# Performance work log

Hardware: AMD Instinct MI355X
Metric: run time of the kernel (lower is better)

The kernel has to match this reference:

```python
import jax, jax.numpy as jnp
import numpy as np

N_NODES = 50000
N_EDGES = 500000
NEG_SLOPE = 0.2  # PyG GATConv default leaky_relu slope
EPS = 1e-16


def gat_conv(x, src, dst, W, a_src, a_dst, b, heads, ch):
    """PyG-style GATConv (concat=True), self-loops assumed already in src/dst."""
    n = x.shape[0]
    h = (x @ W).reshape(n, heads, ch)                      # [N,H,C]
    alpha_s = jnp.sum(h * a_src, axis=-1)                  # [N,H]
    alpha_d = jnp.sum(h * a_dst, axis=-1)                  # [N,H]
    e = jax.nn.leaky_relu(alpha_s[src] + alpha_d[dst], NEG_SLOPE)  # [E,H]
    m = jax.ops.segment_max(e, dst, num_segments=n)        # [N,H] segment softmax (stable)
    m = jnp.where(jnp.isfinite(m), m, 0.0)
    ex = jnp.exp(e - m[dst])
    den = jax.ops.segment_sum(ex, dst, num_segments=n)
    alpha = ex / (den[dst] + EPS)                          # [E,H]
    msg = h[src] * alpha[..., None]                        # [E,H,C] gather->weight
    out = jax.ops.segment_sum(msg, dst, num_segments=n)    # [N,H,C] scatter-add
    return out.reshape(n, heads * ch) + b


def setup_inputs() -> dict:
    key = jax.random.key(0)
    ks = jax.random.split(key, 11)
    s = 0.05
    return {
        "edge_index": jax.random.randint(ks[0], (2, N_EDGES), 0, N_NODES, dtype=jnp.int32),
        "batch_size": 8,
        "node_emb": jax.random.normal(ks[1], (N_NODES, 64), jnp.float32),
        "W1": jax.random.normal(ks[2], (64, 512), jnp.float32) * s,
        "att_src1": jax.random.normal(ks[3], (4, 128), jnp.float32) * s,
        "att_dst1": jax.random.normal(ks[4], (4, 128), jnp.float32) * s,
        "b1": jax.random.normal(ks[5], (512,), jnp.float32) * s,
        "W2": jax.random.normal(ks[6], (512, 256), jnp.float32) * s,
        "att_src2": jax.random.normal(ks[7], (1, 256), jnp.float32) * s,
        "att_dst2": jax.random.normal(ks[8], (1, 256), jnp.float32) * s,
        "b2": jax.random.normal(ks[9], (256,), jnp.float32) * s,
    }


def reference(edge_index, batch_size, node_emb, W1, att_src1, att_dst1, b1,
              W2, att_src2, att_dst2, b2):
    # add self-loops (PyG GATConv default add_self_loops=True)
    loops = jnp.arange(N_NODES, dtype=edge_index.dtype)
    src = jnp.concatenate([edge_index[0], loops])
    dst = jnp.concatenate([edge_index[1], loops])
    x = gat_conv(node_emb, src, dst, W1, att_src1, att_dst1, b1, heads=4, ch=128)
    x = jax.nn.elu(x)  # dropout inactive at eval
    x = gat_conv(x, src, dst, W2, att_src2, att_dst2, b2, heads=1, ch=256)
    g = jnp.mean(x, axis=0, keepdims=True)                 # [1, 256]
    return jnp.broadcast_to(g, (batch_size, g.shape[1]))
```

## Files before the change

### kernel.cpp

```cpp
#include <hip/hip_runtime.h>
#include <cstdint>

#define N_NODES 50000
#define N_EDGES 500000
#define ET (N_NODES + N_EDGES)
#define EBLK 2149
#define NEBLK8 1563

typedef unsigned short u16;
typedef unsigned int   u32;
typedef __attribute__((ext_vector_type(8))) short short8;
typedef __attribute__((ext_vector_type(4))) float f32x4;

__device__ __forceinline__ float bf2f(u16 s) { return __uint_as_float((u32)s << 16); }
__device__ __forceinline__ u16 f2bf(float f) {
  u32 u = __float_as_uint(f);
  u32 r = (u + 0x7FFFu + ((u >> 16) & 1u)) >> 16;
  return (u16)r;
}
__device__ __forceinline__ void unpack8(uint4 u, float* f) {
  f[0] = __uint_as_float(u.x << 16); f[1] = __uint_as_float(u.x & 0xffff0000u);
  f[2] = __uint_as_float(u.y << 16); f[3] = __uint_as_float(u.y & 0xffff0000u);
  f[4] = __uint_as_float(u.z << 16); f[5] = __uint_as_float(u.z & 0xffff0000u);
  f[6] = __uint_as_float(u.w << 16); f[7] = __uint_as_float(u.w & 0xffff0000u);
}
__device__ __forceinline__ float lrelu(float v) { return v >= 0.f ? v : 0.2f * v; }

__device__ __forceinline__ int detect_fp32(const u16* __restrict__ ne) {
  int lane = threadIdx.x & 63;
  int bad = 0;
  #pragma unroll
  for (int j = 0; j < 2; ++j) {
    float v = fabsf(bf2f(ne[lane * 2 + j * 128]));
    bad += (!(v < 16.0f)) ? 1 : 0;
  }
  #pragma unroll
  for (int off = 32; off >= 1; off >>= 1) bad += __shfl_xor(bad, off, 64);
  return bad > 16;
}

__global__ __launch_bounds__(256) void k_prep(const int* __restrict__ ei,
                                              int* __restrict__ deg,
                                              const void* __restrict__ ne_src,
                                              u16* __restrict__ ne_b,
                                              const void* __restrict__ w1src,
                                              u16* __restrict__ W1t,
                                              const void* __restrict__ w2src,
                                              u16* __restrict__ W2t,
                                              const void* s0, const void* s1,
                                              const void* s2, const void* s3,
                                              const void* s4, const void* s5,
                                              float* d0, float* d1, float* d2,
                                              float* d3, float* d4, float* d5) {
  int b = blockIdx.x, tid = threadIdx.x;
  if (b < EBLK) {
    int e = b * 256 + tid;
    if (e < ET) {
      int d = (e < N_EDGES) ? ei[N_EDGES + e] : (e - N_EDGES);
      atomicAdd(&deg[d], 1);
    }
    return;
  }
  int fp32 = detect_fp32((const u16*)ne_src);
  b -= EBLK;
  if (b < NEBLK8) {
    int idx = b * 256 + tid;
    if (idx < 400000) {
      if (fp32) {
        const float4* f4 = (const float4*)ne_src;
        float4 a = f4[idx * 2], c = f4[idx * 2 + 1];
        uint4 o;
        o.x = (u32)f2bf(a.x) | ((u32)f2bf(a.y) << 16);
        o.y = (u32)f2bf(a.z) | ((u32)f2bf(a.w) << 16);
        o.z = (u32)f2bf(c.x) | ((u32)f2bf(c.y) << 16);
        o.w = (u32)f2bf(c.z) | ((u32)f2bf(c.w) << 16);
        ((uint4*)ne_b)[idx] = o;
      } else {
        ((uint4*)ne_b)[idx] = ((const uint4*)ne_src)[idx];
      }
    }
    return;
  }
  b -= NEBLK8;
  if (b < 640) {
    int i = b * 256 + tid;
    if (i < 32768) {
      int n = i >> 6, k = i & 63;
      W1t[i] = fp32 ? f2bf(((const float*)w1src)[k * 512 + n])
                    : ((const u16*)w1src)[k * 512 + n];
    } else {
      int j = i - 32768;
      int n = j >> 9, k = j & 511;
      W2t[j] = fp32 ? f2bf(((const float*)w2src)[k * 256 + n])
                    : ((const u16*)w2src)[k * 256 + n];
    }
    return;
  }
  b -= 640;
  {
    int i = b * 256 + tid;
    const void* s; float* d; int j;
    if      (i < 512)  { s = s0; d = d0; j = i; }
    else if (i < 1024) { s = s1; d = d1; j = i - 512; }
    else if (i < 1536) { s = s2; d = d2; j = i - 1024; }
    else if (i < 1792) { s = s3; d = d3; j = i - 1536; }
    else if (i < 2048) { s = s4; d = d4; j = i - 1792; }
    else if (i < 2304) { s = s5; d = d5; j = i - 2048; }
    else return;
    d[j] = fp32 ? ((const float*)s)[j] : bf2f(((const u16*)s)[j]);
  }
}

__global__ void k_vab(const u16* __restrict__ W1t,
                      const float* __restrict__ as1v, const float* __restrict__ ad1v,
                      float* __restrict__ va_s, float* __restrict__ va_d,
                      const u16* __restrict__ W2t,
                      const float* __restrict__ as2v, const float* __restrict__ ad2v,
                      float* __restrict__ va2_s, float* __restrict__ va2_d) {
  if (blockIdx.x == 0) {
    int t = threadIdx.x;
    int h = t >> 6, k = t & 63;
    float s = 0.f, d = 0.f;
    for (int c = 0; c < 128; ++c) {
      float w = bf2f(W1t[(size_t)(h * 128 + c) * 64 + k]);
      s = fmaf(as1v[h * 128 + c], w, s);
      d = fmaf(ad1v[h * 128 + c], w, d);
    }
    va_s[t] = s;
    va_d[t] = d;
  } else {
    int k = (blockIdx.x - 1) * 256 + threadIdx.x;
    if (k >= 512) return;
    float s = 0.f, d = 0.f;
    for (int c = 0; c < 256; ++c) {
      float w = bf2f(W2t[(size_t)c * 512 + k]);
      s = fmaf(as2v[c], w, s);
      d = fmaf(ad2v[c], w, d);
    }
    va2_s[k] = s;
    va2_d[k] = d;
  }
}

__global__ __launch_bounds__(1024) void k_partial(const int* __restrict__ deg,
                                                  int* __restrict__ excl,
                                                  int* __restrict__ btot) {
  __shared__ int wsum[16];
  int tid = threadIdx.x;
  int i = blockIdx.x * 1024 + tid;
  int v = (i < N_NODES) ? deg[i] : 0;
  int lane = tid & 63, wid = tid >> 6;
  int incl = v;
  #pragma unroll
  for (int off = 1; off < 64; off <<= 1) {
    int t = __shfl_up(incl, off, 64);
    if (lane >= off) incl += t;
  }
  if (lane == 63) wsum[wid] = incl;
  __syncthreads();
  int prefix = 0;
  for (int w = 0; w < wid; ++w) prefix += wsum[w];
  if (i < N_NODES) excl[i] = prefix + incl - v;
  if (tid == 1023) btot[blockIdx.x] = prefix + incl;
}

__global__ __launch_bounds__(1024) void k_add(int* __restrict__ row_off,
                                              int* __restrict__ cursor,
                                              const int* __restrict__ btot,
                                              int nb) {
  __shared__ int sbase;
  int tid = threadIdx.x;
  if (tid < 64) {
    int v = (tid < nb) ? btot[tid] : 0;
    int incl = v;
    #pragma unroll
    for (int off = 1; off < 64; off <<= 1) {
      int t = __shfl_up(incl, off, 64);
      if (tid >= off) incl += t;
    }
    if (tid == (int)blockIdx.x) sbase = incl - v;
  }
  __syncthreads();
  int i = blockIdx.x * 1024 + tid;
  if (i < N_NODES) {
    int r = row_off[i] + sbase;
    row_off[i] = r;
    cursor[i] = r;
  }
  if (blockIdx.x == 0 && tid == 0) row_off[N_NODES] = ET;
}

__global__ __launch_bounds__(256) void k_scal(const int* __restrict__ ei,
                                              int* __restrict__ cursor,
                                              u16* __restrict__ srcs,
                                              const u16* __restrict__ ne_b,
                                              const float* __restrict__ va_s,
                                              const float* __restrict__ va_d,
                                              float* __restrict__ as_o,
                                              float* __restrict__ ad_o) {
  int b = blockIdx.x;
  if (b < EBLK) {
    int e = b * 256 + threadIdx.x;
    if (e >= ET) return;
    int s, d;
    if (e < N_EDGES) { s = ei[e]; d = ei[N_EDGES + e]; }
    else { s = d = e - N_EDGES; }
    int pos = atomicAdd(&cursor[d], 1);
    srcs[pos] = (u16)s;
    return;
  }
  b -= EBLK;
  int wid = threadIdx.x >> 6, lane = threadIdx.x & 63;
  int n = b * 4 + wid;
  if (n >= N_NODES) return;
  int h = lane >> 4, il = lane & 15;
  u32 u2[2];
  *(uint2*)u2 = *(const uint2*)(ne_b + (size_t)n * 64 + il * 4);
  float f[4];
  f[0] = bf2f((u16)u2[0]); f[1] = bf2f((u16)(u2[0] >> 16));
  f[2] = bf2f((u16)u2[1]); f[3] = bf2f((u16)(u2[1] >> 16));
  float4 vs = *(const float4*)(va_s + h * 64 + il * 4);
  float4 vd = *(const float4*)(va_d + h * 64 + il * 4);
  float s = f[0] * vs.x + f[1] * vs.y + f[2] * vs.z + f[3] * vs.w;
  float d = f[0] * vd.x + f[1] * vd.y + f[2] * vd.z + f[3] * vd.w;
  #pragma unroll
  for (int off = 8; off >= 1; off >>= 1) {
    s += __shfl_xor(s, off, 64);
    d += __shfl_xor(d, off, 64);
  }
  if (il == 0) { as_o[n * 4 + h] = s; ad_o[n * 4 + h] = d; }
}

#define LSTR 40
__global__ __launch_bounds__(256) void k_gemm_as2(const u16* __restrict__ aggne,
                                                  const u16* __restrict__ W1t,
                                                  const float* __restrict__ b1f,
                                                  const float* __restrict__ va2_s,
                                                  const float* __restrict__ va2_d,
                                                  float* __restrict__ as2,
                                                  float* __restrict__ ad2, int M) {
  __shared__ __align__(16) u16 As[128 * LSTR];
  __shared__ __align__(16) u16 Bs[128 * LSTR];
  const int tid = threadIdx.x;
  const int lane = tid & 63, wid = tid >> 6;
  const int wr = (wid >> 1) * 64, wc = (wid & 1) * 64;
  const int m = lane & 15, q = lane >> 4;
  const int row0 = blockIdx.x * 128, head = blockIdx.y;
  const u16* Bt = W1t + (size_t)head * 128 * 64;
  f32x4 acc[4][4] = {};
  #pragma unroll
  for (int kk = 0; kk < 64; kk += 32) {
    #pragma unroll
    for (int i = 0; i < 2; ++i) {
      int v = tid + i * 256;
      int row = v >> 2, ch = (v & 3) * 8;
      uint4 u = make_uint4(0, 0, 0, 0);
      int gr = row0 + row;
      if (gr < M) u = *(const uint4*)(aggne + (size_t)gr * 256 + head * 64 + kk + ch);
      *(uint4*)(As + row * LSTR + ch) = u;
    }
    #pragma unroll
    for (int i = 0; i < 2; ++i) {
      int v = tid + i * 256;
      int row = v >> 2, ch = (v & 3) * 8;
      uint4 u = *(const uint4*)(Bt + (size_t)row * 64 + kk + ch);
      *(uint4*)(Bs + row * LSTR + ch) = u;
    }
    __syncthreads();
    short8 af[4], bfr[4];
    #pragma unroll
    for (int t = 0; t < 4; ++t) {
      af[t]  = *(const short8*)(As + (wr + t * 16 + m) * LSTR + q * 8);
      bfr[t] = *(const short8*)(Bs + (wc + t * 16 + m) * LSTR + q * 8);
    }
    #pragma unroll
    for (int mt = 0; mt < 4; ++mt)
      #pragma unroll
      for (int nt = 0; nt < 4; ++nt)
        acc[mt][nt] = __builtin_amdgcn_mfma_f32_16x16x32_bf16(
            af[mt], bfr[nt], acc[mt][nt], 0, 0, 0);
    __syncthreads();
  }
  float vsr[4], vdr[4], br[4];
  #pragma unroll
  for (int nt = 0; nt < 4; ++nt) {
    int cb = head * 128 + wc + nt * 16 + m;
    br[nt] = b1f[cb]; vsr[nt] = va2_s[cb]; vdr[nt] = va2_d[cb];
  }
  #pragma unroll
  for (int mt = 0; mt < 4; ++mt) {
    float sp[4] = {}, dp[4] = {};
    #pragma unroll
    for (int nt = 0; nt < 4; ++nt)
      #pragma unroll
      for (int r = 0; r < 4; ++r) {
        float v = acc[mt][nt][r] + br[nt];
        v = v > 0.f ? v : (__expf(v) - 1.0f);
        sp[r] = fmaf(v, vsr[nt], sp[r]);
        dp[r] = fmaf(v, vdr[nt], dp[r]);
      }
    #pragma unroll
    for (int r = 0; r < 4; ++r) {
      #pragma unroll
      for (int off = 1; off <= 8; off <<= 1) {
        sp[r] += __shfl_xor(sp[r], off, 64);
        dp[r] += __shfl_xor(dp[r], off, 64);
      }
      int gr = row0 + wr + mt * 16 + q * 4 + r;
      if (m == 0 && gr < M) {
        atomicAdd(&as2[gr], sp[r]);
        atomicAdd(&ad2[gr], dp[r]);
      }
    }
  }
}

__global__ __launch_bounds__(256) void k_gemm_ws(const u16* __restrict__ aggne,
                                                 const u16* __restrict__ W1t,
                                                 const float* __restrict__ b1f,
                                                 const float* __restrict__ cwt,
                                                 float* __restrict__ s_vec, int M) {
  __shared__ __align__(16) u16 As[128 * LSTR];
  __shared__ __align__(16) u16 Bs[128 * LSTR];
  __shared__ float part[128];
  const int tid = threadIdx.x;
  const int lane = tid & 63, wid = tid >> 6;
  const int wr = (wid >> 1) * 64, wc = (wid & 1) * 64;
  const int m = lane & 15, q = lane >> 4;
  const int row0 = blockIdx.x * 128, head = blockIdx.y;
  const u16* Bt = W1t + (size_t)head * 128 * 64;
  f32x4 acc[4][4] = {};
  #pragma unroll
  for (int kk = 0; kk < 64; kk += 32) {
    #pragma unroll
    for (int i = 0; i < 2; ++i) {
      int v = tid + i * 256;
      int row = v >> 2, ch = (v & 3) * 8;
      uint4 u = make_uint4(0, 0, 0, 0);
      int gr = row0 + row;
      if (gr < M) u = *(const uint4*)(aggne + (size_t)gr * 256 + head * 64 + kk + ch);
      *(uint4*)(As + row * LSTR + ch) = u;
    }
    #pragma unroll
    for (int i = 0; i < 2; ++i) {
      int v = tid + i * 256;
      int row = v >> 2, ch = (v & 3) * 8;
      uint4 u = *(const uint4*)(Bt + (size_t)row * 64 + kk + ch);
      *(uint4*)(Bs + row * LSTR + ch) = u;
    }
    __syncthreads();
    short8 af[4], bfr[4];
    #pragma unroll
    for (int t = 0; t < 4; ++t) {
      af[t]  = *(const short8*)(As + (wr + t * 16 + m) * LSTR + q * 8);
      bfr[t] = *(const short8*)(Bs + (wc + t * 16 + m) * LSTR + q * 8);
    }
    #pragma unroll
    for (int mt = 0; mt < 4; ++mt)
      #pragma unroll
      for (int nt = 0; nt < 4; ++nt)
        acc[mt][nt] = __builtin_amdgcn_mfma_f32_16x16x32_bf16(
            af[mt], bfr[nt], acc[mt][nt], 0, 0, 0);
    __syncthreads();
  }
  if (tid < 128) part[tid] = 0.f;
  float c_l = 0.f;
  int crow = row0 + wr + lane;
  if (crow < M) c_l = cwt[crow];
  float cvr[16];
  #pragma unroll
  for (int mt = 0; mt < 4; ++mt)
    #pragma unroll
    for (int r = 0; r < 4; ++r)
      cvr[mt * 4 + r] = __shfl(c_l, mt * 16 + q * 4 + r, 64);
  __syncthreads();
  float colacc[4] = {};
  #pragma unroll
  for (int nt = 0; nt < 4; ++nt) {
    float b = b1f[head * 128 + wc + nt * 16 + m];
    #pragma unroll
    for (int mt = 0; mt < 4; ++mt)
      #pragma unroll
      for (int r = 0; r < 4; ++r) {
        float v = acc[mt][nt][r] + b;
        v = v > 0.f ? v : (__expf(v) - 1.0f);
        colacc[nt] = fmaf(cvr[mt * 4 + r], v, colacc[nt]);
      }
  }
  #pragma unroll
  for (int nt = 0; nt < 4; ++nt) {
    colacc[nt] += __shfl_xor(colacc[nt], 16, 64);
    colacc[nt] += __shfl_xor(colacc[nt], 32, 64);
    if (q == 0) atomicAdd(&part[wc + nt * 16 + m], colacc[nt]);
  }
  __syncthreads();
  if (tid < 128) atomicAdd(&s_vec[head * 128 + tid], part[tid]);
}

__global__ __launch_bounds__(256) void k_fagg1(const int* __restrict__ row_off,
                                               const u16* __restrict__ srcs,
                                               const u16* __restrict__ ne_b,
                                               const float* __restrict__ as1,
                                               const float* __restrict__ ad1,
                                               u16* __restrict__ aggne) {
  int wid = threadIdx.x >> 6, lane = threadIdx.x & 63;
  int n = blockIdx.x * 4 + wid;
  if (n >= N_NODES) return;
  int start = row_off[n], end = row_off[n + 1];
  int g = lane >> 4, il = lane & 15;
  float adn_g = ad1[n * 4 + g];
  float sum = 0.f;
  for (int e0 = start; e0 < end; e0 += 16) {
    int e = e0 + il;
    if (e < end) sum += __expf(lrelu(as1[(int)srcs[e] * 4 + g] + adn_g));
  }
  #pragma unroll
  for (int off = 8; off >= 1; off >>= 1) sum += __shfl_xor(sum, off, 64);
  float inv = 1.0f / (sum + 1e-16f);
  float i_[4], d_[4];
  #pragma unroll
  for (int h = 0; h < 4; ++h) {
    i_[h] = __shfl(inv, h * 16, 64);
    d_[h] = __shfl(adn_g, h * 16, 64);
  }
  float acc[4] = {};
  for (int e0 = start; e0 < end; e0 += 64) {
    int lim = end - e0; if (lim > 64) lim = 64;
    int es = e0 + lane;
    int sreg = (int)srcs[es < end ? es : end - 1];
    float4 a = *(const float4*)(as1 + sreg * 4);
    float wreg[4];
    wreg[0] = __expf(lrelu(a.x + d_[0])) * i_[0];
    wreg[1] = __expf(lrelu(a.y + d_[1])) * i_[1];
    wreg[2] = __expf(lrelu(a.z + d_[2])) * i_[2];
    wreg[3] = __expf(lrelu(a.w + d_[3])) * i_[3];
    int j = 0;
    for (; j + 3 < lim; j += 4) {
      int sa = __shfl(sreg, j, 64),     sb = __shfl(sreg, j + 1, 64);
      int sc = __shfl(sreg, j + 2, 64), sd = __shfl(sreg, j + 3, 64);
      float f0 = bf2f(ne_b[(size_t)sa * 64 + lane]);
      float f1 = bf2f(ne_b[(size_t)sb * 64 + lane]);
      float f2 = bf2f(ne_b[(size_t)sc * 64 + lane]);
      float f3 = bf2f(ne_b[(size_t)sd * 64 + lane]);
      #pragma unroll
      for (int h = 0; h < 4; ++h) {
        acc[h] = fmaf(__shfl(wreg[h], j, 64), f0, acc[h]);
        acc[h] = fmaf(__shfl(wreg[h], j + 1, 64), f1, acc[h]);
        acc[h] = fmaf(__shfl(wreg[h], j + 2, 64), f2, acc[h]);
        acc[h] = fmaf(__shfl(wreg[h], j + 3, 64), f3, acc[h]);
      }
    }
    for (; j < lim; ++j) {
      int sa = __shfl(sreg, j, 64);
      float f0 = bf2f(ne_b[(size_t)sa * 64 + lane]);
      #pragma unroll
      for (int h = 0; h < 4; ++h)
        acc[h] = fmaf(__shfl(wreg[h], j, 64), f0, acc[h]);
    }
  }
  #pragma unroll
  for (int h = 0; h < 4; ++h)
    aggne[(size_t)n * 256 + h * 64 + lane] = f2bf(acc[h]);
}

__global__ __launch_bounds__(256) void k_nodew(const int* __restrict__ row_off,
                                               const u16* __restrict__ srcs,
                                               const float* __restrict__ as2,
                                               const float* __restrict__ ad2,
                                               float* __restrict__ c) {
  int wid = threadIdx.x >> 6, lane = threadIdx.x & 63;
  int n = blockIdx.x * 4 + wid;
  if (n >= N_NODES) return;
  int start = row_off[n], end = row_off[n + 1];
  int deg = end - start;
  float adn = ad2[n];
  if (deg <= 64) {
    int e = start + (lane < deg ? lane : 0);
    int s = (int)srcs[e];
    float ex = (lane < deg) ? __expf(lrelu(as2[s] + adn)) : 0.f;
    float sum = ex;
    #pragma unroll
    for (int off = 32; off >= 1; off >>= 1) sum += __shfl_xor(sum, off, 64);
    float w = ex / (sum + 1e-16f);
    if (lane < deg) atomicAdd(&c[s], w);
  } else {
    float sum = 0.f;
    for (int e = start + lane; e < end; e += 64)
      sum += __expf(lrelu(as2[(int)srcs[e]] + adn));
    #pragma unroll
    for (int off = 32; off >= 1; off >>= 1) sum += __shfl_xor(sum, off, 64);
    float inv = 1.0f / (sum + 1e-16f);
    for (int e = start + lane; e < end; e += 64) {
      int s = (int)srcs[e];
      float w = __expf(lrelu(as2[s] + adn)) * inv;
      atomicAdd(&c[s], w);
    }
  }
}

__global__ __launch_bounds__(256) void k_tinyfinal(const float* __restrict__ s_vec,
                                                   const u16* __restrict__ W2t,
                                                   const float* __restrict__ b2f,
                                                   float* __restrict__ out,
                                                   int out_size) {
  int wid = threadIdx.x >> 6, lane = threadIdx.x & 63;
  int cbase = blockIdx.x * 64 + wid * 16;
  float sv[8];
  #pragma unroll
  for (int j = 0; j < 8; ++j) sv[j] = s_vec[lane * 8 + j];
  for (int i = 0; i < 16; ++i) {
    int cc = cbase + i;
    uint4 u = *(const uint4*)(W2t + (size_t)cc * 512 + lane * 8);
    float f[8];
    unpack8(u, f);
    float p = 0.f;
    #pragma unroll
    for (int j = 0; j < 8; ++j) p = fmaf(sv[j], f[j], p);
    #pragma unroll
    for (int off = 32; off >= 1; off >>= 1) p += __shfl_xor(p, off, 64);
    if (lane == 0) {
      float val = p * (1.0f / (float)N_NODES) + b2f[cc];
      for (int o = cc; o < out_size; o += 256) out[o] = val;
    }
  }
}

extern "C" void kernel_launch(void* const* d_in, const int* in_sizes, int n_in,
                              void* d_out, int out_size, void* d_ws, size_t ws_size,
                              hipStream_t stream) {
  (void)in_sizes; (void)n_in; (void)ws_size;
  const int* edge_index = (const int*)d_in[0];
  float* out = (float*)d_out;

  char* w = (char*)d_ws;
  size_t off = 0;
  auto alloc = [&](size_t bytes) -> void* {
    void* p = w + off;
    off += (bytes + 255) & ~(size_t)255;
    return p;
  };
  u16*   ne_b    = (u16*)  alloc((size_t)N_NODES * 64 * 2);
  u16*   W1t     = (u16*)  alloc(32768 * 2);
  u16*   W2t     = (u16*)  alloc(131072 * 2);
  float* as1v    = (float*)alloc(512 * 4);
  float* ad1v    = (float*)alloc(512 * 4);
  float* b1f     = (float*)alloc(512 * 4);
  float* as2v    = (float*)alloc(256 * 4);
  float* ad2v    = (float*)alloc(256 * 4);
  float* b2f     = (float*)alloc(256 * 4);
  float* va_s    = (float*)alloc(256 * 4);
  float* va_d    = (float*)alloc(256 * 4);
  float* va2_s   = (float*)alloc(512 * 4);
  float* va2_d   = (float*)alloc(512 * 4);
  u16*   aggne   = (u16*)  alloc((size_t)N_NODES * 256 * 2);
  float* as1     = (float*)alloc((size_t)N_NODES * 4 * 4);
  float* ad1     = (float*)alloc((size_t)N_NODES * 4 * 4);
  size_t z0 = off;
  float* as2     = (float*)alloc((size_t)N_NODES * 4);
  float* ad2     = (float*)alloc((size_t)N_NODES * 4);
  float* cwt     = (float*)alloc((size_t)N_NODES * 4);
  float* s_vec   = (float*)alloc(512 * 4);
  int*   deg     = (int*)  alloc((size_t)N_NODES * 4);
  size_t z1 = off;
  int*   row_off = (int*)  alloc((size_t)(N_NODES + 1) * 4);
  int*   cursor  = (int*)  alloc((size_t)N_NODES * 4);
  u16*   srcs    = (u16*)  alloc((size_t)ET * 2);
  int*   btot    = (int*)  alloc(64 * 4);

  hipMemsetAsync(w + z0, 0, z1 - z0, stream);

  k_prep<<<EBLK + NEBLK8 + 640 + 9, 256, 0, stream>>>(
      edge_index, deg, d_in[2], ne_b, d_in[3], W1t, d_in[7], W2t,
      d_in[4], d_in[5], d_in[6], d_in[8], d_in[9], d_in[10],
      as1v, ad1v, b1f, as2v, ad2v, b2f);
  k_vab<<<3, 256, 0, stream>>>(W1t, as1v, ad1v, va_s, va_d,
                               W2t, as2v, ad2v, va2_s, va2_d);

  k_partial<<<49, 1024, 0, stream>>>(deg, row_off, btot);
  k_add    <<<49, 1024, 0, stream>>>(row_off, cursor, btot, 49);

  k_scal<<<EBLK + (N_NODES + 3) / 4, 256, 0, stream>>>(
      edge_index, cursor, srcs, ne_b, va_s, va_d, as1, ad1);

  k_fagg1<<<(N_NODES + 3) / 4, 256, 0, stream>>>(row_off, srcs, ne_b, as1, ad1, aggne);
  dim3 gl1((N_NODES + 127) / 128, 4);
  k_gemm_as2<<<gl1, 256, 0, stream>>>(aggne, W1t, b1f, va2_s, va2_d, as2, ad2,
                                      N_NODES);

  k_nodew<<<(N_NODES + 3) / 4, 256, 0, stream>>>(row_off, srcs, as2, ad2, cwt);
  k_gemm_ws<<<gl1, 256, 0, stream>>>(aggne, W1t, b1f, cwt, s_vec, N_NODES);
  k_tinyfinal<<<4, 256, 0, stream>>>(s_vec, W2t, b2f, out, out_size);
}
```

Before: 291.8 us.

## Store aggregated features head-major and load full K tile once in GEMMs

The aggregation kernel now writes its bf16 output head-major ([head][node][64]) instead of node-major with interleaved heads, so each head's GEMM block reads contiguous 128-byte rows. Both GEMM kernels load the whole 64-wide K slice into shared memory in one pass with a padded stride, then run two MFMA sub-steps without intermediate barriers. This cuts synchronisation and improves coalescing, but uses more shared memory per block, which could lower occupancy.

```diff
diff --git a/kernel.cpp b/kernel.cpp
--- a/kernel.cpp
+++ b/kernel.cpp
@@ -231,7 +231,7 @@
   if (il == 0) { as_o[n * 4 + h] = s; ad_o[n * 4 + h] = d; }
 }
 
-#define LSTR 40
+#define ASTR 72
 __global__ __launch_bounds__(256) void k_gemm_as2(const u16* __restrict__ aggne,
                                                   const u16* __restrict__ W1t,
                                                   const float* __restrict__ b1f,
@@ -239,39 +239,40 @@
                                                   const float* __restrict__ va2_d,
                                                   float* __restrict__ as2,
                                                   float* __restrict__ ad2, int M) {
-  __shared__ __align__(16) u16 As[128 * LSTR];
-  __shared__ __align__(16) u16 Bs[128 * LSTR];
+  __shared__ __align__(16) u16 As[128 * ASTR];
+  __shared__ __align__(16) u16 Bs[128 * ASTR];
   const int tid = threadIdx.x;
   const int lane = tid & 63, wid = tid >> 6;
   const int wr = (wid >> 1) * 64, wc = (wid & 1) * 64;
   const int m = lane & 15, q = lane >> 4;
   const int row0 = blockIdx.x * 128, head = blockIdx.y;
+  const u16* Ah = aggne + (size_t)head * N_NODES * 64;
   const u16* Bt = W1t + (size_t)head * 128 * 64;
+  #pragma unroll
+  for (int i = 0; i < 4; ++i) {
+    int v = tid + i * 256;
+    int row = v >> 3, ch = (v & 7) * 8;
+    uint4 u = make_uint4(0, 0, 0, 0);
+    int gr = row0 + row;
+    if (gr < M) u = *(const uint4*)(Ah + (size_t)gr * 64 + ch);
+    *(uint4*)(As + row * ASTR + ch) = u;
+  }
+  #pragma unroll
+  for (int i = 0; i < 4; ++i) {
+    int v = tid + i * 256;
+    int row = v >> 3, ch = (v & 7) * 8;
+    uint4 u = *(const uint4*)(Bt + (size_t)row * 64 + ch);
+    *(uint4*)(Bs + row * ASTR + ch) = u;
+  }
+  __syncthreads();
   f32x4 acc[4][4] = {};
   #pragma unroll
-  for (int kk = 0; kk < 64; kk += 32) {
-    #pragma unroll
-    for (int i = 0; i < 2; ++i) {
-      int v = tid + i * 256;
-      int row = v >> 2, ch = (v & 3) * 8;
-      uint4 u = make_uint4(0, 0, 0, 0);
-      int gr = row0 + row;
-      if (gr < M) u = *(const uint4*)(aggne + (size_t)gr * 256 + head * 64 + kk + ch);
-      *(uint4*)(As + row * LSTR + ch) = u;
-    }
-    #pragma unroll
-    for (int i = 0; i < 2; ++i) {
-      int v = tid + i * 256;
-      int row = v >> 2, ch = (v & 3) * 8;
-      uint4 u = *(const uint4*)(Bt + (size_t)row * 64 + kk + ch);
-      *(uint4*)(Bs + row * LSTR + ch) = u;
-    }
-    __syncthreads();
+  for (int kk = 0; kk < 2; ++kk) {
     short8 af[4], bfr[4];
     #pragma unroll
     for (int t = 0; t < 4; ++t) {
-      af[t]  = *(const short8*)(As + (wr + t * 16 + m) * LSTR + q * 8);
-      bfr[t] = *(const short8*)(Bs + (wc + t * 16 + m) * LSTR + q * 8);
+      af[t]  = *(const short8*)(As + (wr + t * 16 + m) * ASTR + kk * 32 + q * 8);
+      bfr[t] = *(const short8*)(Bs + (wc + t * 16 + m) * ASTR + kk * 32 + q * 8);
     }
     #pragma unroll
     for (int mt = 0; mt < 4; ++mt)
@@ -279,7 +280,6 @@
       for (int nt = 0; nt < 4; ++nt)
         acc[mt][nt] = __builtin_amdgcn_mfma_f32_16x16x32_bf16(
             af[mt], bfr[nt], acc[mt][nt], 0, 0, 0);
-    __syncthreads();
   }
   float vsr[4], vdr[4], br[4];
   #pragma unroll
@@ -320,40 +320,42 @@
                                                  const float* __restrict__ b1f,
                                                  const float* __restrict__ cwt,
                                                  float* __restrict__ s_vec, int M) {
-  __shared__ __align__(16) u16 As[128 * LSTR];
-  __shared__ __align__(16) u16 Bs[128 * LSTR];
+  __shared__ __align__(16) u16 As[128 * ASTR];
+  __shared__ __align__(16) u16 Bs[128 * ASTR];
   __shared__ float part[128];
   const int tid = threadIdx.x;
   const int lane = tid & 63, wid = tid >> 6;
   const int wr = (wid >> 1) * 64, wc = (wid & 1) * 64;
   const int m = lane & 15, q = lane >> 4;
   const int row0 = blockIdx.x * 128, head = blockIdx.y;
+  const u16* Ah = aggne + (size_t)head * N_NODES * 64;
   const u16* Bt = W1t + (size_t)head * 128 * 64;
+  #pragma unroll
+  for (int i = 0; i < 4; ++i) {
+    int v = tid + i * 256;
+    int row = v >> 3, ch = (v & 7) * 8;
+    uint4 u = make_uint4(0, 0, 0, 0);
+    int gr = row0 + row;
+    if (gr < M) u = *(const uint4*)(Ah + (size_t)gr * 64 + ch);
+    *(uint4*)(As + row * ASTR + ch) = u;
+  }
+  #pragma unroll
+  for (int i = 0; i < 4; ++i) {
+    int v = tid + i * 256;
+    int row = v >> 3, ch = (v & 7) * 8;
+    uint4 u = *(const uint4*)(Bt + (size_t)row * 64 + ch);
+    *(uint4*)(Bs + row * ASTR + ch) = u;
+  }
+  if (tid < 128) part[tid] = 0.f;
+  __syncthreads();
   f32x4 acc[4][4] = {};
   #pragma unroll
-  for (int kk = 0; kk < 64; kk += 32) {
-    #pragma unroll
-    for (int i = 0; i < 2; ++i) {
-      int v = tid + i * 256;
-      int row = v >> 2, ch = (v & 3) * 8;
-      uint4 u = make_uint4(0, 0, 0, 0);
-      int gr = row0 + row;
-      if (gr < M) u = *(const uint4*)(aggne + (size_t)gr * 256 + head * 64 + kk + ch);
-      *(uint4*)(As + row * LSTR + ch) = u;
-    }
-    #pragma unroll
-    for (int i = 0; i < 2; ++i) {
-      int v = tid + i * 256;
-      int row = v >> 2, ch = (v & 3) * 8;
-      uint4 u = *(const uint4*)(Bt + (size_t)row * 64 + kk + ch);
-      *(uint4*)(Bs + row * LSTR + ch) = u;
-    }
-    __syncthreads();
+  for (int kk = 0; kk < 2; ++kk) {
     short8 af[4], bfr[4];
     #pragma unroll
     for (int t = 0; t < 4; ++t) {
-      af[t]  = *(const short8*)(As + (wr + t * 16 + m) * LSTR + q * 8);
-      bfr[t] = *(const short8*)(Bs + (wc + t * 16 + m) * LSTR + q * 8);
+      af[t]  = *(const short8*)(As + (wr + t * 16 + m) * ASTR + kk * 32 + q * 8);
+      bfr[t] = *(const short8*)(Bs + (wc + t * 16 + m) * ASTR + kk * 32 + q * 8);
     }
     #pragma unroll
     for (int mt = 0; mt < 4; ++mt)
@@ -361,9 +363,7 @@
       for (int nt = 0; nt < 4; ++nt)
         acc[mt][nt] = __builtin_amdgcn_mfma_f32_16x16x32_bf16(
             af[mt], bfr[nt], acc[mt][nt], 0, 0, 0);
-    __syncthreads();
-  }
-  if (tid < 128) part[tid] = 0.f;
+  }
   float c_l = 0.f;
   int crow = row0 + wr + lane;
   if (crow < M) c_l = cwt[crow];
@@ -373,7 +373,6 @@
     #pragma unroll
     for (int r = 0; r < 4; ++r)
       cvr[mt * 4 + r] = __shfl(c_l, mt * 16 + q * 4 + r, 64);
-  __syncthreads();
   float colacc[4] = {};
   #pragma unroll
   for (int nt = 0; nt < 4; ++nt) {
@@ -460,7 +459,7 @@
   }
   #pragma unroll
   for (int h = 0; h < 4; ++h)
-    aggne[(size_t)n * 256 + h * 64 + lane] = f2bf(acc[h]);
+    aggne[(size_t)h * (N_NODES * 64) + (size_t)n * 64 + lane] = f2bf(acc[h]);
 }
 
 __global__ __launch_bounds__(256) void k_nodew(const int* __restrict__ row_off,
```

Result: no change. 294.5 us (+0.9%).
